# Kernel tuning notes

Hardware: AMD Instinct MI355X
Metric: run time of the kernel (lower is better)

Reference implementation:

```python
import jax, jax.numpy as jnp
import numpy as np

B, S, D, E = 2, 2048, 1024, 16  # batch, cutoff (seq), dmodel, n_experts


def setup_inputs() -> dict:
    key = jax.random.key(0)
    k = jax.random.split(key, 6)
    scale = 1.0 / np.sqrt(D)
    return {
        "x": jax.random.normal(k[0], (B, S, D), dtype=jnp.float32),
        "gate": jax.random.normal(k[1], (D, E), dtype=jnp.float32) * scale,
        "W1": jax.random.normal(k[2], (E, D, D), dtype=jnp.float32) * scale,  # lin1: Linear(dmodel, dmodel*E), split per expert
        "b1": jnp.zeros((E, D), dtype=jnp.float32),
        "W2": jax.random.normal(k[3], (E, D, D), dtype=jnp.float32) * scale,  # lin2: Linear(dmodel*E, dmodel), split per expert
        "b2": jnp.zeros((D,), dtype=jnp.float32),
        "topk": 256,
    }


def reference(x, gate, W1, b1, W2, b2, topk):
    # Expert-choice gating: softmax over the token (cutoff) axis per expert.
    logits = jnp.einsum("bsd,de->bse", x, gate)            # (B, S, E)
    probs = jax.nn.softmax(logits, axis=1)                  # softmax over tokens
    # Each expert selects its top-k tokens.
    g, idx = jax.lax.top_k(jnp.swapaxes(probs, 1, 2), topk)  # (B, E, k)
    # Gather selected tokens: (B, E, k, D)
    xin = jnp.take_along_axis(x[:, None, :, :], idx[..., None], axis=2)
    # Per-expert 2-layer FFN (hidden size = dmodel, per width = dmodel*n_experts)
    h = jax.nn.relu(jnp.einsum("bekd,edf->bekf", xin, W1) + b1[None, :, None, :])
    out = jnp.einsum("bekf,efd->bekd", h, W2) + b2           # (B, E, k, D)
    weighted = out * g[..., None]
    # Scatter-add back to token positions.
    y = jnp.zeros_like(x)
    b_idx = jnp.arange(x.shape[0])[:, None, None]            # (B, 1, 1)
    y = y.at[b_idx, idx].add(weighted)
    return y
```

## Files before the change

### kernel.cpp

```cpp
#include <hip/hip_runtime.h>
#include <stdint.h>
#include <math.h>

constexpr int CB = 2;
constexpr int CS = 2048;
constexpr int CD = 1024;
constexpr int CE = 16;
constexpr int CK = 256;

typedef short bf16x8 __attribute__((ext_vector_type(8)));
typedef float f32x4 __attribute__((ext_vector_type(4)));

typedef __attribute__((address_space(1))) const unsigned int gu32;
typedef __attribute__((address_space(3))) unsigned int lu32;
typedef __attribute__((address_space(3))) unsigned short lds_us;

__device__ __forceinline__ void async16(const void* g, lds_us* l) {
    __builtin_amdgcn_global_load_lds((gu32*)g, (lu32*)l, 16, 0, 0);
}

__device__ __forceinline__ bf16x8 ds_read128(const lds_us* p) {
    bf16x8 v;
    asm volatile("ds_read_b128 %0, %1" : "=v"(v) : "v"(p));
    return v;
}

__device__ inline unsigned short f2bf(float f) {
    union { float f; uint32_t u; } v; v.f = f;
    uint32_t u = v.u;
    uint32_t r = (u + 0x7FFFu + ((u >> 16) & 1u)) >> 16;
    return (unsigned short)r;
}

__global__ __launch_bounds__(256)
void logits_part_kernel(const float* __restrict__ x,
                        const float* __restrict__ gate,
                        float* __restrict__ part) {
    const int tt = blockIdx.x;
    const int dt = blockIdx.y;
    const int tid = threadIdx.x;

    __shared__ float Xs[256 * 17];

    float acc[CE];
#pragma unroll
    for (int e = 0; e < CE; e++) acc[e] = 0.0f;

    const int tokl = tid >> 2;
    const int c4 = (tid & 3) << 2;

    for (int dch = 0; dch < 4; dch++) {
        const int dbase = dt * 64 + dch * 16;
        __syncthreads();
#pragma unroll
        for (int q = 0; q < 4; q++) {
            const int tok = q * 64 + tokl;
            const f32x4 v = *(const f32x4*)(x + ((size_t)(tt * 256 + tok)) * CD + dbase + c4);
            Xs[tok * 17 + c4 + 0] = v[0];
            Xs[tok * 17 + c4 + 1] = v[1];
            Xs[tok * 17 + c4 + 2] = v[2];
            Xs[tok * 17 + c4 + 3] = v[3];
        }
        __syncthreads();
#pragma unroll
        for (int d = 0; d < 16; d++) {
            const float xv = Xs[tid * 17 + d];
            const float* gr = gate + (size_t)(dbase + d) * CE;
#pragma unroll
            for (int e = 0; e < CE; e++) acc[e] = fmaf(xv, gr[e], acc[e]);
        }
    }
    float* pr = part + ((size_t)dt * (CB * CS) + tt * 256 + tid) * CE;
#pragma unroll
    for (int e = 0; e < CE; e++) pr[e] = acc[e];
}

__global__ __launch_bounds__(256)
void logits_reduce_kernel(const float* __restrict__ part,
                          float* __restrict__ logits) {
    const int i = blockIdx.x * 256 + threadIdx.x;
    float s = 0.0f;
#pragma unroll
    for (int p = 0; p < 16; p++) s += part[(size_t)p * (CB * CS * CE) + i];
    logits[i] = s;
}

__global__ void topk_kernel(const float* __restrict__ logits,
                            int* __restrict__ idx_out,
                            float* __restrict__ g_out) {
    const int be = blockIdx.x;
    const int b = be >> 4, e = be & 15;
    const int tid = threadIdx.x;
    const int lane = tid & 63, wid = tid >> 6;

    __shared__ float redf[4];
    __shared__ int hist[256];
    __shared__ int wsum[4];
    __shared__ int sh_bin, sh_rank;
    __shared__ int scnt, eqc;
    __shared__ int eqbuf[CS];

    float lv[8], p[8];
    unsigned int uv[8];
#pragma unroll
    for (int j = 0; j < 8; j++) {
        const int s = tid + j * 256;
        lv[j] = logits[((size_t)(b * CS + s)) * CE + e];
    }
    float m = lv[0];
#pragma unroll
    for (int j = 1; j < 8; j++) m = fmaxf(m, lv[j]);
#pragma unroll
    for (int o = 32; o > 0; o >>= 1) m = fmaxf(m, __shfl_down(m, o));
    if (lane == 0) redf[wid] = m;
    __syncthreads();
    m = fmaxf(fmaxf(redf[0], redf[1]), fmaxf(redf[2], redf[3]));
    __syncthreads();
    float lsum = 0.0f;
#pragma unroll
    for (int j = 0; j < 8; j++) {
        p[j] = expf(lv[j] - m);
        uv[j] = __float_as_uint(p[j]);
        lsum += p[j];
    }
#pragma unroll
    for (int o = 32; o > 0; o >>= 1) lsum += __shfl_down(lsum, o);
    if (lane == 0) redf[wid] = lsum;
    __syncthreads();
    const float total = redf[0] + redf[1] + redf[2] + redf[3];
    const float inv_total = 1.0f / total;

    unsigned int prefix = 0;
    int kneed = CK;
    for (int pass = 0; pass < 4; pass++) {
        const int shift = 24 - 8 * pass;
        __syncthreads();
        hist[tid] = 0;
        __syncthreads();
        const unsigned int hmask = (pass == 0) ? 0u : (0xFFFFFFFFu << (shift + 8));
#pragma unroll
        for (int j = 0; j < 8; j++)
            if ((uv[j] & hmask) == prefix)
                atomicAdd(&hist[(uv[j] >> shift) & 255], 1);
        __syncthreads();
        const int own = hist[tid];
        int s = own;
#pragma unroll
        for (int o = 1; o < 64; o <<= 1) {
            int t = __shfl_down(s, o);
            if (lane + o < 64) s += t;
        }
        if (lane == 0) wsum[wid] = s;
        __syncthreads();
        int above = 0;
        for (int ww = wid + 1; ww < 4; ww++) above += wsum[ww];
        const int incl = s + above;
        if (incl >= kneed && (incl - own) < kneed) {
            sh_bin = tid;
            sh_rank = kneed - (incl - own);
        }
        __syncthreads();
        prefix |= ((unsigned int)sh_bin) << shift;
        kneed = sh_rank;
    }
    const unsigned int v = prefix;
    const int quota = kneed;

    if (tid == 0) { scnt = 0; eqc = 0; }
    __syncthreads();
#pragma unroll
    for (int j = 0; j < 8; j++) {
        const int s = tid + j * 256;
        if (uv[j] > v) {
            const int pos = atomicAdd(&scnt, 1);
            idx_out[be * CK + pos] = s;
            g_out[be * CK + pos] = p[j] * inv_total;
        } else if (uv[j] == v) {
            const int pos = atomicAdd(&eqc, 1);
            eqbuf[pos] = s;
        }
    }
    __syncthreads();
    if (tid == 0) {
        const int cgt = scnt;
        const int n = eqc;
        const float gv = __uint_as_float(v) * inv_total;
        if (n > quota) {
            for (int i = 0; i < quota; i++) {
                int mn = i;
                for (int k2 = i + 1; k2 < n; k2++)
                    if (eqbuf[k2] < eqbuf[mn]) mn = k2;
                const int t2 = eqbuf[i]; eqbuf[i] = eqbuf[mn]; eqbuf[mn] = t2;
            }
        }
        for (int i = 0; i < quota; i++) {
            idx_out[be * CK + cgt + i] = eqbuf[i];
            g_out[be * CK + cgt + i] = gv;
        }
    }
}

__global__ void gather_kernel(const float* __restrict__ x,
                              const int* __restrict__ idx_ws,
                              unsigned short* __restrict__ xinbuf) {
    const int row = blockIdx.x;
    const int be = row >> 8;
    const int b = be >> 4;
    const int tok = idx_ws[row];
    const int c0 = threadIdx.x * 4;
    const f32x4 f = *(const f32x4*)(x + ((size_t)b * CS + tok) * CD + c0);
    union { unsigned short u[4]; uint2 v; } t;
    t.u[0] = f2bf(f[0]); t.u[1] = f2bf(f[1]); t.u[2] = f2bf(f[2]); t.u[3] = f2bf(f[3]);
    *(uint2*)(xinbuf + (size_t)row * CD + c0) = t.v;
}

__global__ __launch_bounds__(256)
void wt_kernel(const float* __restrict__ W, unsigned short* __restrict__ Wt) {
    const int kt = blockIdx.x, nt = blockIdx.y, e = blockIdx.z;
    const float* src = W + (size_t)e * CD * CD;
    unsigned short* dst = Wt + (size_t)e * CD * CD;
    const int tid = threadIdx.x;
    __shared__ unsigned short T[64 * 64];

    const int kr = tid >> 4;
    const int n4 = (tid & 15) << 2;
#pragma unroll
    for (int it = 0; it < 4; it++) {
        const int k = it * 16 + kr;
        const f32x4 v = *(const f32x4*)(src + (size_t)(kt * 64 + k) * CD + nt * 64 + n4);
        const int pp = k >> 4;
        const int klo = k & 15;
#pragma unroll
        for (int i = 0; i < 4; i++) {
            const int n = n4 + i;
            T[n * 64 + ((pp ^ ((n >> 2) & 3)) << 4) + klo] = f2bf(v[i]);
        }
    }
    __syncthreads();
    const int n = tid >> 2;
    const int pp = tid & 3;
    const int sw = pp ^ ((n >> 2) & 3);
    const uint4 a = *(const uint4*)&T[n * 64 + (sw << 4)];
    const uint4 b = *(const uint4*)&T[n * 64 + (sw << 4) + 8];
    unsigned short* drow = dst + (size_t)(nt * 64 + n) * CD + kt * 64 + pp * 16;
    *(uint4*)drow = a;
    *(uint4*)(drow + 8) = b;
}

template <int PHASE>
__global__ __launch_bounds__(256, 2)
void ffn_gemm(const unsigned short* __restrict__ Ain,
              const unsigned short* __restrict__ Wt,
              const float* __restrict__ bias,
              unsigned short* __restrict__ hout,
              const int* __restrict__ idx_ws,
              const float* __restrict__ g_ws,
              float* __restrict__ y) {
    const int id = blockIdx.x;
    const int e = (id & 7) | (((id >> 3) & 1) << 3);
    const int b = (id >> 4) & 1;
    const int mtile = (id >> 5) & 1;
    const int ntile = id >> 6;
    const int be = b * 16 + e;
    const int tid = threadIdx.x;
    const int w = tid >> 6, l = tid & 63;
    const int wm = w & 1, wn = w >> 1;
    const int quad = l >> 4, lr = l & 15;

    __shared__ __align__(16) unsigned short As_s[3][128 * 32];
    __shared__ __align__(16) unsigned short Bs_s[3][128 * 32];

    f32x4 acc[4][4];
    const f32x4 zz = {0.f, 0.f, 0.f, 0.f};
#pragma unroll
    for (int mi = 0; mi < 4; mi++)
#pragma unroll
        for (int ni = 0; ni < 4; ni++) acc[mi][ni] = zz;

    const unsigned short* Abase = Ain + ((size_t)be * CK + mtile * 128) * CD;
    const unsigned short* Bbase = Wt + ((size_t)e * CD + ntile * 128) * CD;

    int c_c[2];
    size_t goff[2];
#pragma unroll
    for (int j = 0; j < 2; j++) {
        const int c = (w + j * 4) * 64 + l;
        c_c[j] = c;
        const int row = c >> 2;
        const int kc = (c & 3) ^ ((row >> 1) & 3);
        goff[j] = (size_t)row * CD + kc * 8;
    }

    const int fpos = (quad ^ ((lr >> 1) & 3)) * 8;

    lds_us* pa0 = (lds_us*)As_s[0]; lds_us* pa1 = (lds_us*)As_s[1]; lds_us* pa2 = (lds_us*)As_s[2];
    lds_us* pb0 = (lds_us*)Bs_s[0]; lds_us* pb1 = (lds_us*)Bs_s[1]; lds_us* pb2 = (lds_us*)Bs_s[2];

#pragma unroll
    for (int j = 0; j < 2; j++) {
        async16(Abase + goff[j], pa0 + c_c[j] * 8);
        async16(Bbase + goff[j], pb0 + c_c[j] * 8);
    }
#pragma unroll
    for (int j = 0; j < 2; j++) {
        async16(Abase + goff[j] + 32, pa1 + c_c[j] * 8);
        async16(Bbase + goff[j] + 32, pb1 + c_c[j] * 8);
    }

    for (int ks = 0; ks < 32; ks++) {
        if (ks < 30) {
            const int k2 = (ks + 2) * 32;
#pragma unroll
            for (int j = 0; j < 2; j++) {
                async16(Abase + goff[j] + k2, pa2 + c_c[j] * 8);
                async16(Bbase + goff[j] + k2, pb2 + c_c[j] * 8);
            }
            asm volatile("s_waitcnt vmcnt(8)" ::: "memory");
        } else if (ks == 30) {
            asm volatile("s_waitcnt vmcnt(4)" ::: "memory");
        } else {
            asm volatile("s_waitcnt vmcnt(0)" ::: "memory");
        }
        asm volatile("s_barrier" ::: "memory");

        bf16x8 af[4], bfr[4];
#pragma unroll
        for (int mi = 0; mi < 4; mi++)
            af[mi] = ds_read128(pa0 + (wm * 64 + mi * 16 + lr) * 32 + fpos);
#pragma unroll
        for (int ni = 0; ni < 4; ni++)
            bfr[ni] = ds_read128(pb0 + (wn * 64 + ni * 16 + lr) * 32 + fpos);
        asm volatile("s_waitcnt lgkmcnt(0)"
                     : "+v"(af[0]), "+v"(af[1]), "+v"(af[2]), "+v"(af[3]),
                       "+v"(bfr[0]), "+v"(bfr[1]), "+v"(bfr[2]), "+v"(bfr[3])
                     :: "memory");
#pragma unroll
        for (int mi = 0; mi < 4; mi++)
#pragma unroll
            for (int ni = 0; ni < 4; ni++)
                acc[mi][ni] = __builtin_amdgcn_mfma_f32_16x16x32_bf16(
                    af[mi], bfr[ni], acc[mi][ni], 0, 0, 0);

        asm volatile("s_barrier" ::: "memory");
        lds_us* t = pa0; pa0 = pa1; pa1 = pa2; pa2 = t;
        t = pb0; pb0 = pb1; pb1 = pb2; pb2 = t;
    }

    const int gn_base = ntile * 128 + wn * 64;
    if (PHASE == 0) {
#pragma unroll
        for (int mi = 0; mi < 4; mi++)
#pragma unroll
            for (int r = 0; r < 4; r++) {
                const int slot = mtile * 128 + wm * 64 + mi * 16 + quad * 4 + r;
                unsigned short* outrow = hout + ((size_t)be * CK + slot) * CD;
#pragma unroll
                for (int ni = 0; ni < 4; ni++) {
                    const int col = gn_base + ni * 16 + lr;
                    float hv = acc[mi][ni][r] + bias[e * CD + col];
                    hv = fmaxf(hv, 0.0f);
                    outrow[col] = f2bf(hv);
                }
            }
    } else {
#pragma unroll
        for (int mi = 0; mi < 4; mi++)
#pragma unroll
            for (int r = 0; r < 4; r++) {
                const int slot = mtile * 128 + wm * 64 + mi * 16 + quad * 4 + r;
                const int tok = idx_ws[be * CK + slot];
                const float gval = g_ws[be * CK + slot];
                float* yrow = y + ((size_t)b * CS + tok) * CD;
#pragma unroll
                for (int ni = 0; ni < 4; ni++) {
                    const int col = gn_base + ni * 16 + lr;
                    const float val = (acc[mi][ni][r] + bias[col]) * gval;
                    atomicAdd(&yrow[col], val);
                }
            }
    }
}

extern "C" void kernel_launch(void* const* d_in, const int* in_sizes, int n_in,
                              void* d_out, int out_size, void* d_ws, size_t ws_size,
                              hipStream_t stream) {
    const float* x    = (const float*)d_in[0];
    const float* gate = (const float*)d_in[1];
    const float* W1   = (const float*)d_in[2];
    const float* b1   = (const float*)d_in[3];
    const float* W2   = (const float*)d_in[4];
    const float* b2   = (const float*)d_in[5];
    float* y = (float*)d_out;

    char* ws = (char*)d_ws;
    float* logits = (float*)ws;
    int* idxw = (int*)(ws + 262144);
    float* gw = (float*)(ws + 294912);
    unsigned short* xinbuf = (unsigned short*)(ws + 327680);
    unsigned short* hbuf = (unsigned short*)(ws + 17104896);
    float* partbuf = (float*)(ws + 17104896);
    unsigned short* wtbuf = (unsigned short*)(ws + 33882112);

    logits_part_kernel<<<dim3(16, 16), 256, 0, stream>>>(x, gate, partbuf);
    logits_reduce_kernel<<<CB * CS * CE / 256, 256, 0, stream>>>(partbuf, logits);
    topk_kernel<<<CB * CE, 256, 0, stream>>>(logits, idxw, gw);
    gather_kernel<<<CB * CE * CK, 256, 0, stream>>>(x, idxw, xinbuf);
    wt_kernel<<<dim3(16, 16, CE), 256, 0, stream>>>(W1, wtbuf);
    hipMemsetAsync(d_out, 0, (size_t)CB * CS * CD * sizeof(float), stream);
    ffn_gemm<0><<<512, 256, 0, stream>>>(xinbuf, wtbuf, b1, hbuf, idxw, gw, y);
    wt_kernel<<<dim3(16, 16, CE), 256, 0, stream>>>(W2, wtbuf);
    ffn_gemm<1><<<512, 256, 0, stream>>>(hbuf, wtbuf, b2, nullptr, idxw, gw, y);
}
```

Before: 283.1 us.

## Enlarge FFN GEMM tile to 256x128 with 8 waves and BK=64 pipeline

The expert FFN GEMM now has each 512-thread block compute a full 256-row expert tile against 128 output columns, with a K step of 64 and a triple-buffered LDS pipeline. Global prefetches are split across four sub-steps and interleaved with MFMA groups under raised wave priority. The aim is more operand reuse per LDS load and better overlap of loads with MFMA work. In exchange, LDS use grows to about 147KB, which allows only one block per CU, and the grid shrinks to 256 blocks.

```diff
diff --git a/kernel.cpp b/kernel.cpp
--- a/kernel.cpp
+++ b/kernel.cpp
@@ -247,8 +247,10 @@
     *(uint4*)(drow + 8) = b;
 }
 
+#define MFMA16(A_, B_, C_) __builtin_amdgcn_mfma_f32_16x16x32_bf16((A_), (B_), (C_), 0, 0, 0)
+
 template <int PHASE>
-__global__ __launch_bounds__(256, 2)
+__global__ __launch_bounds__(512, 2)
 void ffn_gemm(const unsigned short* __restrict__ Ain,
               const unsigned short* __restrict__ Wt,
               const float* __restrict__ bias,
@@ -257,18 +259,19 @@
               const float* __restrict__ g_ws,
               float* __restrict__ y) {
     const int id = blockIdx.x;
-    const int e = (id & 7) | (((id >> 3) & 1) << 3);
-    const int b = (id >> 4) & 1;
-    const int mtile = (id >> 5) & 1;
-    const int ntile = id >> 6;
-    const int be = b * 16 + e;
+    const int xcd = id & 7;
+    const int q = id >> 3;
+    const int e = ((q & 1) << 3) | xcd;
+    const int b = (q >> 1) & 1;
+    const int ntile = q >> 2;
+    const int be = b * CE + e;
     const int tid = threadIdx.x;
     const int w = tid >> 6, l = tid & 63;
-    const int wm = w & 1, wn = w >> 1;
+    const int wm = w >> 1, wn = w & 1;
     const int quad = l >> 4, lr = l & 15;
 
-    __shared__ __align__(16) unsigned short As_s[3][128 * 32];
-    __shared__ __align__(16) unsigned short Bs_s[3][128 * 32];
+    __shared__ __align__(16) unsigned short LA[3][256 * 64];
+    __shared__ __align__(16) unsigned short LB[3][128 * 64];
 
     f32x4 acc[4][4];
     const f32x4 zz = {0.f, 0.f, 0.f, 0.f};
@@ -277,73 +280,144 @@
 #pragma unroll
         for (int ni = 0; ni < 4; ni++) acc[mi][ni] = zz;
 
-    const unsigned short* Abase = Ain + ((size_t)be * CK + mtile * 128) * CD;
-    const unsigned short* Bbase = Wt + ((size_t)e * CD + ntile * 128) * CD;
-
-    int c_c[2];
-    size_t goff[2];
+    const unsigned short* Agb = Ain + (size_t)be * CK * CD;
+    const unsigned short* Bgb = Wt + ((size_t)e * CD + ntile * 128) * CD;
+
+    const unsigned short* pAg[4]; int dA[4];
+#pragma unroll
+    for (int j = 0; j < 4; j++) {
+        const int u = w * 256 + j * 64 + l;
+        const int row = u >> 3;
+        const int c = (u & 7) ^ (row & 7);
+        pAg[j] = Agb + (size_t)row * CD + c * 8;
+        dA[j] = u * 8;
+    }
+    const unsigned short* pBg[2]; int dB[2];
 #pragma unroll
     for (int j = 0; j < 2; j++) {
-        const int c = (w + j * 4) * 64 + l;
-        c_c[j] = c;
-        const int row = c >> 2;
-        const int kc = (c & 3) ^ ((row >> 1) & 3);
-        goff[j] = (size_t)row * CD + kc * 8;
-    }
-
-    const int fpos = (quad ^ ((lr >> 1) & 3)) * 8;
-
-    lds_us* pa0 = (lds_us*)As_s[0]; lds_us* pa1 = (lds_us*)As_s[1]; lds_us* pa2 = (lds_us*)As_s[2];
-    lds_us* pb0 = (lds_us*)Bs_s[0]; lds_us* pb1 = (lds_us*)Bs_s[1]; lds_us* pb2 = (lds_us*)Bs_s[2];
-
-#pragma unroll
-    for (int j = 0; j < 2; j++) {
-        async16(Abase + goff[j], pa0 + c_c[j] * 8);
-        async16(Bbase + goff[j], pb0 + c_c[j] * 8);
-    }
-#pragma unroll
-    for (int j = 0; j < 2; j++) {
-        async16(Abase + goff[j] + 32, pa1 + c_c[j] * 8);
-        async16(Bbase + goff[j] + 32, pb1 + c_c[j] * 8);
-    }
-
-    for (int ks = 0; ks < 32; ks++) {
-        if (ks < 30) {
-            const int k2 = (ks + 2) * 32;
-#pragma unroll
-            for (int j = 0; j < 2; j++) {
-                async16(Abase + goff[j] + k2, pa2 + c_c[j] * 8);
-                async16(Bbase + goff[j] + k2, pb2 + c_c[j] * 8);
-            }
-            asm volatile("s_waitcnt vmcnt(8)" ::: "memory");
-        } else if (ks == 30) {
-            asm volatile("s_waitcnt vmcnt(4)" ::: "memory");
-        } else {
-            asm volatile("s_waitcnt vmcnt(0)" ::: "memory");
-        }
-        asm volatile("s_barrier" ::: "memory");
-
-        bf16x8 af[4], bfr[4];
-#pragma unroll
-        for (int mi = 0; mi < 4; mi++)
-            af[mi] = ds_read128(pa0 + (wm * 64 + mi * 16 + lr) * 32 + fpos);
-#pragma unroll
-        for (int ni = 0; ni < 4; ni++)
-            bfr[ni] = ds_read128(pb0 + (wn * 64 + ni * 16 + lr) * 32 + fpos);
+        const int u = w * 128 + j * 64 + l;
+        const int row = u >> 3;
+        const int c = (u & 7) ^ (row & 7);
+        pBg[j] = Bgb + (size_t)row * CD + c * 8;
+        dB[j] = u * 8;
+    }
+
+    const int sc0 = (quad ^ (lr & 7)) * 8;
+    const int sc1 = ((quad ^ (lr & 7)) ^ 4) * 8;
+    int offA[2][4], offB[2][4];
+#pragma unroll
+    for (int mi = 0; mi < 4; mi++) {
+        const int r = wm * 64 + mi * 16 + lr;
+        offA[0][mi] = r * 64 + sc0;
+        offA[1][mi] = r * 64 + sc1;
+    }
+#pragma unroll
+    for (int ni = 0; ni < 4; ni++) {
+        const int r = wn * 64 + ni * 16 + lr;
+        offB[0][ni] = r * 64 + sc0;
+        offB[1][ni] = r * 64 + sc1;
+    }
+
+    lds_us* pA0 = (lds_us*)LA[0]; lds_us* pA1 = (lds_us*)LA[1]; lds_us* pA2 = (lds_us*)LA[2];
+    lds_us* pB0 = (lds_us*)LB[0]; lds_us* pB1 = (lds_us*)LB[1]; lds_us* pB2 = (lds_us*)LB[2];
+
+#pragma unroll
+    for (int j = 0; j < 4; j++) async16(pAg[j], pA0 + dA[j]);
+#pragma unroll
+    for (int j = 0; j < 2; j++) async16(pBg[j], pB0 + dB[j]);
+#pragma unroll
+    for (int j = 0; j < 4; j++) async16(pAg[j] + 64, pA1 + dA[j]);
+#pragma unroll
+    for (int j = 0; j < 2; j++) async16(pBg[j] + 64, pB1 + dB[j]);
+    asm volatile("s_waitcnt vmcnt(6)" ::: "memory");
+    asm volatile("s_barrier" ::: "memory");
+
+    for (int t = 0; t < 16; t++) {
+        const bool pf = (t + 2) < 16;
+        const int kel = (t + 2) * 64;
+        bf16x8 a0, a1, a2, a3, b0, b1, b2, b3;
+
+        a0 = ds_read128(pA0 + offA[0][0]);
+        a1 = ds_read128(pA0 + offA[0][1]);
+        a2 = ds_read128(pA0 + offA[0][2]);
+        a3 = ds_read128(pA0 + offA[0][3]);
+        b0 = ds_read128(pB0 + offB[0][0]);
+        b1 = ds_read128(pB0 + offB[0][1]);
+        if (pf) { async16(pAg[0] + kel, pA2 + dA[0]); async16(pAg[1] + kel, pA2 + dA[1]); }
+        asm volatile("s_barrier" ::: "memory");
         asm volatile("s_waitcnt lgkmcnt(0)"
-                     : "+v"(af[0]), "+v"(af[1]), "+v"(af[2]), "+v"(af[3]),
-                       "+v"(bfr[0]), "+v"(bfr[1]), "+v"(bfr[2]), "+v"(bfr[3])
-                     :: "memory");
-#pragma unroll
-        for (int mi = 0; mi < 4; mi++)
-#pragma unroll
-            for (int ni = 0; ni < 4; ni++)
-                acc[mi][ni] = __builtin_amdgcn_mfma_f32_16x16x32_bf16(
-                    af[mi], bfr[ni], acc[mi][ni], 0, 0, 0);
-
-        asm volatile("s_barrier" ::: "memory");
-        lds_us* t = pa0; pa0 = pa1; pa1 = pa2; pa2 = t;
-        t = pb0; pb0 = pb1; pb1 = pb2; pb2 = t;
+                     : "+v"(a0), "+v"(a1), "+v"(a2), "+v"(a3), "+v"(b0), "+v"(b1) :: "memory");
+        __builtin_amdgcn_s_setprio(1);
+        acc[0][0] = MFMA16(a0, b0, acc[0][0]);
+        acc[1][0] = MFMA16(a1, b0, acc[1][0]);
+        acc[2][0] = MFMA16(a2, b0, acc[2][0]);
+        acc[3][0] = MFMA16(a3, b0, acc[3][0]);
+        acc[0][1] = MFMA16(a0, b1, acc[0][1]);
+        acc[1][1] = MFMA16(a1, b1, acc[1][1]);
+        acc[2][1] = MFMA16(a2, b1, acc[2][1]);
+        acc[3][1] = MFMA16(a3, b1, acc[3][1]);
+        __builtin_amdgcn_s_setprio(0);
+        asm volatile("s_barrier" ::: "memory");
+
+        b2 = ds_read128(pB0 + offB[0][2]);
+        b3 = ds_read128(pB0 + offB[0][3]);
+        if (pf) { async16(pAg[2] + kel, pA2 + dA[2]); async16(pAg[3] + kel, pA2 + dA[3]); }
+        asm volatile("s_barrier" ::: "memory");
+        asm volatile("s_waitcnt lgkmcnt(0)" : "+v"(b2), "+v"(b3) :: "memory");
+        __builtin_amdgcn_s_setprio(1);
+        acc[0][2] = MFMA16(a0, b2, acc[0][2]);
+        acc[1][2] = MFMA16(a1, b2, acc[1][2]);
+        acc[2][2] = MFMA16(a2, b2, acc[2][2]);
+        acc[3][2] = MFMA16(a3, b2, acc[3][2]);
+        acc[0][3] = MFMA16(a0, b3, acc[0][3]);
+        acc[1][3] = MFMA16(a1, b3, acc[1][3]);
+        acc[2][3] = MFMA16(a2, b3, acc[2][3]);
+        acc[3][3] = MFMA16(a3, b3, acc[3][3]);
+        __builtin_amdgcn_s_setprio(0);
+        asm volatile("s_barrier" ::: "memory");
+
+        a0 = ds_read128(pA0 + offA[1][0]);
+        a1 = ds_read128(pA0 + offA[1][1]);
+        a2 = ds_read128(pA0 + offA[1][2]);
+        a3 = ds_read128(pA0 + offA[1][3]);
+        b0 = ds_read128(pB0 + offB[1][0]);
+        b1 = ds_read128(pB0 + offB[1][1]);
+        if (pf) { async16(pBg[0] + kel, pB2 + dB[0]); async16(pBg[1] + kel, pB2 + dB[1]); }
+        asm volatile("s_barrier" ::: "memory");
+        asm volatile("s_waitcnt lgkmcnt(0)"
+                     : "+v"(a0), "+v"(a1), "+v"(a2), "+v"(a3), "+v"(b0), "+v"(b1) :: "memory");
+        __builtin_amdgcn_s_setprio(1);
+        acc[0][0] = MFMA16(a0, b0, acc[0][0]);
+        acc[1][0] = MFMA16(a1, b0, acc[1][0]);
+        acc[2][0] = MFMA16(a2, b0, acc[2][0]);
+        acc[3][0] = MFMA16(a3, b0, acc[3][0]);
+        acc[0][1] = MFMA16(a0, b1, acc[0][1]);
+        acc[1][1] = MFMA16(a1, b1, acc[1][1]);
+        acc[2][1] = MFMA16(a2, b1, acc[2][1]);
+        acc[3][1] = MFMA16(a3, b1, acc[3][1]);
+        __builtin_amdgcn_s_setprio(0);
+        asm volatile("s_barrier" ::: "memory");
+
+        b2 = ds_read128(pB0 + offB[1][2]);
+        b3 = ds_read128(pB0 + offB[1][3]);
+        asm volatile("s_barrier" ::: "memory");
+        asm volatile("s_waitcnt lgkmcnt(0)" : "+v"(b2), "+v"(b3) :: "memory");
+        __builtin_amdgcn_s_setprio(1);
+        acc[0][2] = MFMA16(a0, b2, acc[0][2]);
+        acc[1][2] = MFMA16(a1, b2, acc[1][2]);
+        acc[2][2] = MFMA16(a2, b2, acc[2][2]);
+        acc[3][2] = MFMA16(a3, b2, acc[3][2]);
+        acc[0][3] = MFMA16(a0, b3, acc[0][3]);
+        acc[1][3] = MFMA16(a1, b3, acc[1][3]);
+        acc[2][3] = MFMA16(a2, b3, acc[2][3]);
+        acc[3][3] = MFMA16(a3, b3, acc[3][3]);
+        __builtin_amdgcn_s_setprio(0);
+        if (t < 14)       asm volatile("s_waitcnt vmcnt(6)" ::: "memory");
+        else if (t == 14) asm volatile("s_waitcnt vmcnt(0)" ::: "memory");
+        asm volatile("s_barrier" ::: "memory");
+
+        lds_us* tp = pA0; pA0 = pA1; pA1 = pA2; pA2 = tp;
+        tp = pB0; pB0 = pB1; pB1 = pB2; pB2 = tp;
     }
 
     const int gn_base = ntile * 128 + wn * 64;
@@ -352,7 +426,7 @@
         for (int mi = 0; mi < 4; mi++)
 #pragma unroll
             for (int r = 0; r < 4; r++) {
-                const int slot = mtile * 128 + wm * 64 + mi * 16 + quad * 4 + r;
+                const int slot = wm * 64 + mi * 16 + quad * 4 + r;
                 unsigned short* outrow = hout + ((size_t)be * CK + slot) * CD;
 #pragma unroll
                 for (int ni = 0; ni < 4; ni++) {
@@ -367,7 +441,7 @@
         for (int mi = 0; mi < 4; mi++)
 #pragma unroll
             for (int r = 0; r < 4; r++) {
-                const int slot = mtile * 128 + wm * 64 + mi * 16 + quad * 4 + r;
+                const int slot = wm * 64 + mi * 16 + quad * 4 + r;
                 const int tok = idx_ws[be * CK + slot];
                 const float gval = g_ws[be * CK + slot];
                 float* yrow = y + ((size_t)b * CS + tok) * CD;
@@ -407,7 +481,7 @@
     gather_kernel<<<CB * CE * CK, 256, 0, stream>>>(x, idxw, xinbuf);
     wt_kernel<<<dim3(16, 16, CE), 256, 0, stream>>>(W1, wtbuf);
     hipMemsetAsync(d_out, 0, (size_t)CB * CS * CD * sizeof(float), stream);
-    ffn_gemm<0><<<512, 256, 0, stream>>>(xinbuf, wtbuf, b1, hbuf, idxw, gw, y);
+    ffn_gemm<0><<<256, 512, 0, stream>>>(xinbuf, wtbuf, b1, hbuf, idxw, gw, y);
     wt_kernel<<<dim3(16, 16, CE), 256, 0, stream>>>(W2, wtbuf);
-    ffn_gemm<1><<<512, 256, 0, stream>>>(hbuf, wtbuf, b2, nullptr, idxw, gw, y);
-}
+    ffn_gemm<1><<<256, 512, 0, stream>>>(hbuf, wtbuf, b2, nullptr, idxw, gw, y);
+}
```

Measured after the change: 282.0 us. No clear change (-0.4%).
